# Performance work log

Hardware: AMD Instinct MI355X
Metric: run time of the kernel (lower is better)

## Reference

```python
import jax, jax.numpy as jnp
import numpy as np

N = 5_000_000   # hits
D = 6           # track-parameter dim (MSE sums over dim=1)
P = 50_000      # max particle_id (0 = noise)


def setup_inputs() -> dict:
    key = jax.random.key(0)
    ks = jax.random.split(key, 8)
    return {
        "W": jax.random.normal(ks[0], (N,), dtype=jnp.float32),
        "beta": jax.random.uniform(ks[1], (N,), dtype=jnp.float32, minval=1e-4, maxval=1.0 - 1e-4),
        "H": jax.random.normal(ks[2], (N, 8), dtype=jnp.float32),
        "pred": jax.random.normal(ks[3], (N, D), dtype=jnp.float32),
        "Y": jax.random.normal(ks[4], (N,), dtype=jnp.float32),
        "particle_id": jax.random.randint(ks[5], (N,), 0, P),
        "track_params": jax.random.normal(ks[6], (N, D), dtype=jnp.float32),
        "reconstructable": jax.random.randint(ks[7], (N,), 0, 2),
    }


def reference(W, beta, H, pred, Y, particle_id, track_params, reconstructable):
    # mask = reconstructable > 0 ; then object_loss on the masked subset.
    # Original loops over unique pids > 0; for each pid the contribution is
    # weight * sum(mse * M * pid) with weight = 1/sum(M * pid) == mean(mse over group).
    # Final: 100 * sum_over_groups(group_mean_mse) / num_groups.
    # We express it as one segment reduce over pid, weighting out
    # non-reconstructable hits and noise (pid == 0).
    mask = reconstructable > 0
    valid = mask & (particle_id > 0)
    w = valid.astype(pred.dtype)                                  # [N]
    mse = jnp.sum((pred - track_params) ** 2, axis=1)             # [N]
    sums = jax.ops.segment_sum(mse * w, particle_id, num_segments=P)   # [P]
    counts = jax.ops.segment_sum(w, particle_id, num_segments=P)       # [P]
    present = counts > 0
    means = jnp.where(present, sums / jnp.where(present, counts, 1.0), 0.0)
    K = jnp.sum(present).astype(pred.dtype)
    return 100.0 * jnp.sum(means) / K
```

## Files before the change

kernel.cpp:

```cpp
#include <hip/hip_runtime.h>

#define PMAX   50000
#define NB     196
#define BPB    256
#define OVFN   (NB * BPB)
#define CAP    32
#define GCAP   16384
#define PACK_C 16777216.0
#define P1_THREADS 512
#define P1_BLOCKS  512
#define T_HITS     4096

#define CTRL_BYTES 406528
#define WS_NEED_BUCKETS (CTRL_BYTES + (size_t)NB * GCAP * 8)

__device__ __forceinline__ float mse6(const float* __restrict__ pred,
                                      const float* __restrict__ tp, int i) {
    const float2* p2 = reinterpret_cast<const float2*>(pred) + (size_t)i * 3;
    const float2* t2 = reinterpret_cast<const float2*>(tp)   + (size_t)i * 3;
    float2 a0 = p2[0], a1 = p2[1], a2 = p2[2];
    float2 b0 = t2[0], b1 = t2[1], b2 = t2[2];
    float d0 = a0.x - b0.x, d1 = a0.y - b0.y, d2 = a1.x - b1.x;
    float d3 = a1.y - b1.y, d4 = a2.x - b2.x, d5 = a2.y - b2.y;
    return d0*d0 + d1*d1 + d2*d2 + d3*d3 + d4*d4 + d5*d5;
}

__global__ __launch_bounds__(P1_THREADS) void
objloss_scatter(const float* __restrict__ pred,
                const float* __restrict__ tp,
                const int* __restrict__ pid,
                const int* __restrict__ recon,
                unsigned long long* __restrict__ gbuf,
                unsigned* __restrict__ gcount,
                double* __restrict__ ovf,
                int n) {
    __shared__ unsigned long long s_buf[NB * CAP];
    __shared__ unsigned s_cnt[NB];
    __shared__ unsigned s_base[NB];

    const int tid  = threadIdx.x;
    const int lane = tid & 63;
    const int wid  = tid >> 6;

    int ntiles = (n + T_HITS - 1) / T_HITS;
    for (int tile = blockIdx.x; tile < ntiles; tile += gridDim.x) {
        for (int b = tid; b < NB; b += P1_THREADS) s_cnt[b] = 0u;
        __syncthreads();

        int base_i = tile * T_HITS;
        #pragma unroll
        for (int h = 0; h < T_HITS / P1_THREADS; ++h) {
            int i = base_i + h * P1_THREADS + tid;
            if (i < n) {
                int p = pid[i];
                int r = recon[i];
                if ((r > 0) & (p > 0) & (p < PMAX)) {
                    float m = mse6(pred, tp, i);
                    int b = p >> 8;
                    unsigned long long e =
                        ((unsigned long long)(unsigned)p << 32) | __float_as_uint(m);
                    unsigned idx = atomicAdd(&s_cnt[b], 1u);
                    if (idx < CAP) s_buf[b * CAP + idx] = e;
                    else atomicAdd(&ovf[p], (double)m + PACK_C);
                }
            }
        }
        __syncthreads();

        if (tid < NB) {
            unsigned c = s_cnt[tid]; if (c > CAP) c = CAP;
            s_base[tid] = c ? atomicAdd(&gcount[tid], c) : 0u;
        }
        __syncthreads();

        for (int b = wid; b < NB; b += 8) {
            unsigned c = s_cnt[b]; if (c > CAP) c = CAP;
            if (c && (unsigned)lane < c) {
                unsigned long long e = s_buf[b * CAP + lane];
                unsigned slot = s_base[b] + (unsigned)lane;
                if (slot < GCAP) {
                    gbuf[(size_t)b * GCAP + slot] = e;
                } else {
                    unsigned p = (unsigned)(e >> 32);
                    atomicAdd(&ovf[p], (double)__uint_as_float((unsigned)e) + PACK_C);
                }
            }
        }
        __syncthreads();
    }
}

__global__ __launch_bounds__(256) void
objloss_accum_dev(const float* __restrict__ pred,
                  const float* __restrict__ tp,
                  const int* __restrict__ pid,
                  const int* __restrict__ recon,
                  double* __restrict__ ovf,
                  int n) {
    int i = blockIdx.x * blockDim.x + threadIdx.x;
    int base = i * 2;
    if (base >= n) return;
    int lim = (base + 2 <= n) ? 2 : 1;
    for (int k = 0; k < lim; ++k) {
        int p = pid[base + k];
        int r = recon[base + k];
        if ((r > 0) & (p > 0) & (p < PMAX)) {
            float m = mse6(pred, tp, base + k);
            atomicAdd(&ovf[p], (double)m + PACK_C);
        }
    }
}

__global__ __launch_bounds__(256) void
objloss_gather(const unsigned long long* __restrict__ gbuf,
               const unsigned* __restrict__ gcount,
               const double* __restrict__ ovf,
               double* __restrict__ partials) {
    __shared__ double s_bins[BPB];
    int b = blockIdx.x;
    int t = threadIdx.x;
    s_bins[t] = 0.0;
    __syncthreads();

    unsigned c = gcount[b]; if (c > GCAP) c = GCAP;
    for (unsigned k = t; k < c; k += 256) {
        unsigned long long e = gbuf[(size_t)b * GCAP + k];
        float m = __uint_as_float((unsigned)e);
        atomicAdd(&s_bins[(unsigned)(e >> 32) & 255u], (double)m + PACK_C);
    }
    __syncthreads();

    double v = s_bins[t] + ovf[(b << 8) | t];
    double lsum = 0.0, lk = 0.0;
    double cnt = floor(v * (1.0 / PACK_C));
    if (cnt > 0.0) { lsum = (v - cnt * PACK_C) / cnt; lk = 1.0; }

    #pragma unroll
    for (int off = 32; off > 0; off >>= 1) {
        lsum += __shfl_down(lsum, off);
        lk   += __shfl_down(lk, off);
    }
    __shared__ double ss[4], sk[4];
    int w = t >> 6, lane = t & 63;
    if (lane == 0) { ss[w] = lsum; sk[w] = lk; }
    __syncthreads();
    if (t == 0) {
        double s = 0.0, k = 0.0;
        #pragma unroll
        for (int j = 0; j < 4; ++j) { s += ss[j]; k += sk[j]; }
        partials[2 * b]     = s;
        partials[2 * b + 1] = k;
    }
}

__global__ __launch_bounds__(256) void
objloss_final(const double* __restrict__ partials, float* __restrict__ out) {
    int t = threadIdx.x;
    double ls = 0.0, lk = 0.0;
    if (t < NB) { ls = partials[2 * t]; lk = partials[2 * t + 1]; }
    #pragma unroll
    for (int off = 32; off > 0; off >>= 1) {
        ls += __shfl_down(ls, off);
        lk += __shfl_down(lk, off);
    }
    __shared__ double ss[4], sk[4];
    int w = t >> 6, lane = t & 63;
    if (lane == 0) { ss[w] = ls; sk[w] = lk; }
    __syncthreads();
    if (t == 0) {
        double s = 0.0, k = 0.0;
        #pragma unroll
        for (int j = 0; j < 4; ++j) { s += ss[j]; k += sk[j]; }
        out[0] = (k > 0.0) ? (float)(100.0 * s / k) : 0.0f;
    }
}

extern "C" void kernel_launch(void* const* d_in, const int* in_sizes, int n_in,
                              void* d_out, int out_size, void* d_ws, size_t ws_size,
                              hipStream_t stream) {
    const float* pred  = (const float*)d_in[3];
    const int*   pid   = (const int*)  d_in[5];
    const float* tp    = (const float*)d_in[6];
    const int*   recon = (const int*)  d_in[7];
    int n = in_sizes[0];

    char* ws = (char*)d_ws;
    double*             ovf      = (double*)ws;
    unsigned*           gcount   = (unsigned*)(ws + 401408);
    double*             partials = (double*)(ws + 402432);
    unsigned long long* gbuf     = (unsigned long long*)(ws + CTRL_BYTES);

    hipMemsetAsync(d_ws, 0, CTRL_BYTES, stream);

    bool buckets = (ws_size >= WS_NEED_BUCKETS);
    if (buckets) {
        objloss_scatter<<<P1_BLOCKS, P1_THREADS, 0, stream>>>(
            pred, tp, pid, recon, gbuf, gcount, ovf, n);
    } else {
        int pairs = (n + 1) / 2;
        objloss_accum_dev<<<(pairs + 255) / 256, 256, 0, stream>>>(
            pred, tp, pid, recon, ovf, n);
    }
    objloss_gather<<<NB, 256, 0, stream>>>(gbuf, gcount, ovf, partials);
    objloss_final<<<1, 256, 0, stream>>>(partials, (float*)d_out);
}
```

Baseline: 425.7 us.

## Pack bucket entries into 32 bits and vectorize two-hit loads per thread

```diff
diff --git a/kernel.cpp b/kernel.cpp
--- a/kernel.cpp
+++ b/kernel.cpp
@@ -3,26 +3,17 @@
 #define PMAX   50000
 #define NB     196
 #define BPB    256
-#define OVFN   (NB * BPB)
-#define CAP    32
+#define CAP    40
 #define GCAP   16384
 #define PACK_C 16777216.0
+#define T_HITS 8192
 #define P1_THREADS 512
-#define P1_BLOCKS  512
-#define T_HITS     4096
 
 #define CTRL_BYTES 406528
-#define WS_NEED_BUCKETS (CTRL_BYTES + (size_t)NB * GCAP * 8)
-
-__device__ __forceinline__ float mse6(const float* __restrict__ pred,
-                                      const float* __restrict__ tp, int i) {
-    const float2* p2 = reinterpret_cast<const float2*>(pred) + (size_t)i * 3;
-    const float2* t2 = reinterpret_cast<const float2*>(tp)   + (size_t)i * 3;
-    float2 a0 = p2[0], a1 = p2[1], a2 = p2[2];
-    float2 b0 = t2[0], b1 = t2[1], b2 = t2[2];
-    float d0 = a0.x - b0.x, d1 = a0.y - b0.y, d2 = a1.x - b1.x;
-    float d3 = a1.y - b1.y, d4 = a2.x - b2.x, d5 = a2.y - b2.y;
-    return d0*d0 + d1*d1 + d2*d2 + d3*d3 + d4*d4 + d5*d5;
+#define WS_NEED_BUCKETS (CTRL_BYTES + (size_t)NB * GCAP * 4)
+
+__device__ __forceinline__ unsigned make_entry(float m, int p) {
+    return (__float_as_uint(m) & 0xFFFFFF00u) | ((unsigned)p & 0xFFu);
 }
 
 __global__ __launch_bounds__(P1_THREADS) void
@@ -30,11 +21,11 @@
                 const float* __restrict__ tp,
                 const int* __restrict__ pid,
                 const int* __restrict__ recon,
-                unsigned long long* __restrict__ gbuf,
+                unsigned* __restrict__ gbuf,
                 unsigned* __restrict__ gcount,
                 double* __restrict__ ovf,
                 int n) {
-    __shared__ unsigned long long s_buf[NB * CAP];
+    __shared__ unsigned s_buf[NB * CAP];
     __shared__ unsigned s_cnt[NB];
     __shared__ unsigned s_base[NB];
 
@@ -42,51 +33,77 @@
     const int lane = tid & 63;
     const int wid  = tid >> 6;
 
-    int ntiles = (n + T_HITS - 1) / T_HITS;
-    for (int tile = blockIdx.x; tile < ntiles; tile += gridDim.x) {
-        for (int b = tid; b < NB; b += P1_THREADS) s_cnt[b] = 0u;
-        __syncthreads();
-
-        int base_i = tile * T_HITS;
-        #pragma unroll
-        for (int h = 0; h < T_HITS / P1_THREADS; ++h) {
-            int i = base_i + h * P1_THREADS + tid;
-            if (i < n) {
-                int p = pid[i];
-                int r = recon[i];
-                if ((r > 0) & (p > 0) & (p < PMAX)) {
-                    float m = mse6(pred, tp, i);
-                    int b = p >> 8;
-                    unsigned long long e =
-                        ((unsigned long long)(unsigned)p << 32) | __float_as_uint(m);
-                    unsigned idx = atomicAdd(&s_cnt[b], 1u);
-                    if (idx < CAP) s_buf[b * CAP + idx] = e;
-                    else atomicAdd(&ovf[p], (double)m + PACK_C);
-                }
+    for (int b = tid; b < NB; b += P1_THREADS) s_cnt[b] = 0u;
+    __syncthreads();
+
+    const long tile0 = (long)blockIdx.x * T_HITS;
+
+    #pragma unroll
+    for (int k = 0; k < T_HITS / (2 * P1_THREADS); ++k) {
+        long base = tile0 + (long)(k * P1_THREADS + tid) * 2;
+        if (base + 1 < n) {
+            int2 pp = *reinterpret_cast<const int2*>(pid + base);
+            int2 rr = *reinterpret_cast<const int2*>(recon + base);
+            const float4* pa = reinterpret_cast<const float4*>(pred + base * 6);
+            const float4* tb = reinterpret_cast<const float4*>(tp   + base * 6);
+            float4 a0 = pa[0], a1 = pa[1], a2 = pa[2];
+            float4 b0 = tb[0], b1 = tb[1], b2 = tb[2];
+
+            float e0 = a0.x - b0.x, e1 = a0.y - b0.y, e2 = a0.z - b0.z;
+            float e3 = a0.w - b0.w, e4 = a1.x - b1.x, e5 = a1.y - b1.y;
+            float m0 = e0*e0 + e1*e1 + e2*e2 + e3*e3 + e4*e4 + e5*e5;
+
+            float f0 = a1.z - b1.z, f1 = a1.w - b1.w, f2 = a2.x - b2.x;
+            float f3 = a2.y - b2.y, f4 = a2.z - b2.z, f5 = a2.w - b2.w;
+            float m1 = f0*f0 + f1*f1 + f2*f2 + f3*f3 + f4*f4 + f5*f5;
+
+            if ((rr.x > 0) & (pp.x > 0) & (pp.x < PMAX)) {
+                unsigned b = (unsigned)pp.x >> 8;
+                unsigned idx = atomicAdd(&s_cnt[b], 1u);
+                if (idx < CAP) s_buf[b * CAP + idx] = make_entry(m0, pp.x);
+                else atomicAdd(&ovf[pp.x], (double)m0 + PACK_C);
+            }
+            if ((rr.y > 0) & (pp.y > 0) & (pp.y < PMAX)) {
+                unsigned b = (unsigned)pp.y >> 8;
+                unsigned idx = atomicAdd(&s_cnt[b], 1u);
+                if (idx < CAP) s_buf[b * CAP + idx] = make_entry(m1, pp.y);
+                else atomicAdd(&ovf[pp.y], (double)m1 + PACK_C);
+            }
+        } else if (base < n) {
+            int p = pid[base];
+            int r = recon[base];
+            if ((r > 0) & (p > 0) & (p < PMAX)) {
+                const float2* p2 = reinterpret_cast<const float2*>(pred) + base * 3;
+                const float2* t2 = reinterpret_cast<const float2*>(tp)   + base * 3;
+                float2 x0 = p2[0], x1 = p2[1], x2 = p2[2];
+                float2 y0 = t2[0], y1 = t2[1], y2 = t2[2];
+                float d0 = x0.x - y0.x, d1 = x0.y - y0.y, d2 = x1.x - y1.x;
+                float d3 = x1.y - y1.y, d4 = x2.x - y2.x, d5 = x2.y - y2.y;
+                float m = d0*d0 + d1*d1 + d2*d2 + d3*d3 + d4*d4 + d5*d5;
+                atomicAdd(&ovf[p], (double)m + PACK_C);
             }
         }
-        __syncthreads();
-
-        if (tid < NB) {
-            unsigned c = s_cnt[tid]; if (c > CAP) c = CAP;
-            s_base[tid] = c ? atomicAdd(&gcount[tid], c) : 0u;
+    }
+    __syncthreads();
+
+    if (tid < NB) {
+        unsigned c = s_cnt[tid]; if (c > CAP) c = CAP;
+        s_base[tid] = c ? atomicAdd(&gcount[tid], c) : 0u;
+    }
+    __syncthreads();
+
+    for (int b = wid; b < NB; b += 8) {
+        unsigned c = s_cnt[b]; if (c > CAP) c = CAP;
+        if ((unsigned)lane < c) {
+            unsigned e = s_buf[b * CAP + lane];
+            unsigned slot = s_base[b] + (unsigned)lane;
+            if (slot < GCAP) {
+                gbuf[(size_t)b * GCAP + slot] = e;
+            } else {
+                unsigned p = ((unsigned)b << 8) | (e & 0xFFu);
+                atomicAdd(&ovf[p], (double)__uint_as_float(e & 0xFFFFFF00u) + PACK_C);
+            }
         }
-        __syncthreads();
-
-        for (int b = wid; b < NB; b += 8) {
-            unsigned c = s_cnt[b]; if (c > CAP) c = CAP;
-            if (c && (unsigned)lane < c) {
-                unsigned long long e = s_buf[b * CAP + lane];
-                unsigned slot = s_base[b] + (unsigned)lane;
-                if (slot < GCAP) {
-                    gbuf[(size_t)b * GCAP + slot] = e;
-                } else {
-                    unsigned p = (unsigned)(e >> 32);
-                    atomicAdd(&ovf[p], (double)__uint_as_float((unsigned)e) + PACK_C);
-                }
-            }
-        }
-        __syncthreads();
     }
 }
 
@@ -98,21 +115,27 @@
                   double* __restrict__ ovf,
                   int n) {
     int i = blockIdx.x * blockDim.x + threadIdx.x;
-    int base = i * 2;
+    long base = (long)i * 2;
     if (base >= n) return;
     int lim = (base + 2 <= n) ? 2 : 1;
     for (int k = 0; k < lim; ++k) {
         int p = pid[base + k];
         int r = recon[base + k];
         if ((r > 0) & (p > 0) & (p < PMAX)) {
-            float m = mse6(pred, tp, base + k);
+            const float2* p2 = reinterpret_cast<const float2*>(pred) + (base + k) * 3;
+            const float2* t2 = reinterpret_cast<const float2*>(tp)   + (base + k) * 3;
+            float2 x0 = p2[0], x1 = p2[1], x2 = p2[2];
+            float2 y0 = t2[0], y1 = t2[1], y2 = t2[2];
+            float d0 = x0.x - y0.x, d1 = x0.y - y0.y, d2 = x1.x - y1.x;
+            float d3 = x1.y - y1.y, d4 = x2.x - y2.x, d5 = x2.y - y2.y;
+            float m = d0*d0 + d1*d1 + d2*d2 + d3*d3 + d4*d4 + d5*d5;
             atomicAdd(&ovf[p], (double)m + PACK_C);
         }
     }
 }
 
 __global__ __launch_bounds__(256) void
-objloss_gather(const unsigned long long* __restrict__ gbuf,
+objloss_gather(const unsigned* __restrict__ gbuf,
                const unsigned* __restrict__ gcount,
                const double* __restrict__ ovf,
                double* __restrict__ partials) {
@@ -124,9 +147,9 @@
 
     unsigned c = gcount[b]; if (c > GCAP) c = GCAP;
     for (unsigned k = t; k < c; k += 256) {
-        unsigned long long e = gbuf[(size_t)b * GCAP + k];
-        float m = __uint_as_float((unsigned)e);
-        atomicAdd(&s_bins[(unsigned)(e >> 32) & 255u], (double)m + PACK_C);
+        unsigned e = gbuf[(size_t)b * GCAP + k];
+        float m = __uint_as_float(e & 0xFFFFFF00u);
+        atomicAdd(&s_bins[e & 0xFFu], (double)m + PACK_C);
     }
     __syncthreads();
 
@@ -185,16 +208,17 @@
     int n = in_sizes[0];
 
     char* ws = (char*)d_ws;
-    double*             ovf      = (double*)ws;
-    unsigned*           gcount   = (unsigned*)(ws + 401408);
-    double*             partials = (double*)(ws + 402432);
-    unsigned long long* gbuf     = (unsigned long long*)(ws + CTRL_BYTES);
+    double*   ovf      = (double*)ws;
+    unsigned* gcount   = (unsigned*)(ws + 401408);
+    double*   partials = (double*)(ws + 402432);
+    unsigned* gbuf     = (unsigned*)(ws + CTRL_BYTES);
 
     hipMemsetAsync(d_ws, 0, CTRL_BYTES, stream);
 
     bool buckets = (ws_size >= WS_NEED_BUCKETS);
     if (buckets) {
-        objloss_scatter<<<P1_BLOCKS, P1_THREADS, 0, stream>>>(
+        int ntiles = (n + T_HITS - 1) / T_HITS;
+        objloss_scatter<<<ntiles, P1_THREADS, 0, stream>>>(
             pred, tp, pid, recon, gbuf, gcount, ovf, n);
     } else {
         int pairs = (n + 1) / 2;
```

New measurement: 421.1 us. No clear change (-1.1%).
